# Optimization experiments

Hardware: AMD Instinct MI355X
Metric: run time of the kernel (lower is better)

The kernel has to match this reference:

```python
import jax, jax.numpy as jnp
import numpy as np

N = 100000          # nodes
E = 3200000         # edges
C_IN = 64
HIDDEN = 64
NUM_CLASSES = 10
NUM_GRAPHS = 256
EPS = 1e-5


def _graph_conv(x, src, dst, w_rel, w_root, b):
    # PyG GraphConv(aggr='mean'): out_i = W_rel * mean_{j->i} x_j + W_root * x_i + b
    msg_sum = jax.ops.segment_sum(x[src], dst, num_segments=N)            # [N, C]
    cnt = jax.ops.segment_sum(jnp.ones((src.shape[0], 1), x.dtype), dst,
                              num_segments=N)                             # [N, 1]
    agg = msg_sum / jnp.maximum(cnt, 1.0)
    return agg @ w_rel + x @ w_root + b


def _batch_norm(x, gamma, beta):
    # PyG BatchNorm in training mode: batch stats over the node dimension
    mean = jnp.mean(x, axis=0)
    var = jnp.var(x, axis=0)
    return (x - mean) * jax.lax.rsqrt(var + EPS) * gamma + beta


def setup_inputs() -> dict:
    key = jax.random.key(0)
    ks = jax.random.split(key, 20)
    x = jax.random.normal(ks[0], (N, C_IN), dtype=jnp.float32)
    edge_index = jax.random.randint(ks[1], (2, E), 0, N, dtype=jnp.int32)
    batch = jnp.sort(jax.random.randint(ks[2], (N,), 0, NUM_GRAPHS, dtype=jnp.int32))

    def lin(k, fan_in, fan_out):
        s = 1.0 / np.sqrt(fan_in)
        return jax.random.uniform(k, (fan_in, fan_out), jnp.float32, -s, s)

    dims = [(C_IN, 16), (16, 32), (32, 32), (32, HIDDEN)]
    params = {}
    ki = 3
    for i, (ci, co) in enumerate(dims, start=1):
        params[f"w_rel{i}"] = lin(ks[ki], ci, co); ki += 1
        params[f"w_root{i}"] = lin(ks[ki], ci, co); ki += 1
        params[f"b{i}"] = jnp.zeros((co,), jnp.float32)
        params[f"g{i}"] = jnp.ones((co,), jnp.float32)
        params[f"be{i}"] = jnp.zeros((co,), jnp.float32)
    params["w_lin1"] = lin(ks[ki], HIDDEN, HIDDEN); ki += 1
    params["b_lin1"] = jnp.zeros((HIDDEN,), jnp.float32)
    params["w_lin2"] = lin(ks[ki], HIDDEN, NUM_CLASSES); ki += 1
    params["b_lin2"] = jnp.zeros((NUM_CLASSES,), jnp.float32)

    return {"x": x, "edge_index": edge_index, "batch": batch, **params}


def reference(x, edge_index, batch,
              w_rel1, w_root1, b1, g1, be1,
              w_rel2, w_root2, b2, g2, be2,
              w_rel3, w_root3, b3, g3, be3,
              w_rel4, w_root4, b4, g4, be4,
              w_lin1, b_lin1, w_lin2, b_lin2):
    src, dst = edge_index[0], edge_index[1]
    h = jax.nn.elu(_batch_norm(_graph_conv(x, src, dst, w_rel1, w_root1, b1), g1, be1))
    h = jax.nn.elu(_batch_norm(_graph_conv(h, src, dst, w_rel2, w_root2, b2), g2, be2))
    h = jax.nn.elu(_batch_norm(_graph_conv(h, src, dst, w_rel3, w_root3, b3), g3, be3))
    h = jax.nn.elu(_batch_norm(_graph_conv(h, src, dst, w_rel4, w_root4, b4), g4, be4))
    # global mean pool over graphs
    pooled = jax.ops.segment_sum(h, batch, num_segments=NUM_GRAPHS)
    cnt = jax.ops.segment_sum(jnp.ones((N, 1), h.dtype), batch, num_segments=NUM_GRAPHS)
    pooled = pooled / jnp.maximum(cnt, 1.0)
    z = jax.nn.relu(pooled @ w_lin1 + b_lin1)
    # dropout omitted (deterministic / eval mode)
    logits = z @ w_lin2 + b_lin2
    return jax.nn.log_softmax(logits, axis=-1)
```

## Files before the change

### kernel.cpp

```cpp
#include <hip/hip_runtime.h>
#include <hip/hip_bf16.h>
#include <math.h>

#define NGRAPHS 256
#define BSHIFT 8
#define NBUCK 512
#define NSORT 256
#define LSTAT 1024
#define GCHUNK 1024
#define SMASK 0x00FFFFFFu

__device__ __forceinline__ float bf2f(unsigned short u) {
    return __uint_as_float((unsigned)u << 16);
}
__device__ __forceinline__ unsigned short f2bf(float f) {
    unsigned u = __float_as_uint(f);
    unsigned r = (u + 0x7FFFu + ((u >> 16) & 1u)) >> 16;
    return (unsigned short)r;
}

__global__ __launch_bounds__(256) void k_bhist(const int* __restrict__ dst, int* __restrict__ hmat, int E,
                                               const float* __restrict__ x, const float* __restrict__ w_rel1,
                                               unsigned short* __restrict__ y1b,
                                               int* __restrict__ colpos, int N) {
    int bid = blockIdx.x, tid = threadIdx.x;
    if (bid < NSORT) {
        __shared__ int hist[NBUCK];
        for (int i = tid; i < NBUCK; i += 256) hist[i] = 0;
        __syncthreads();
        int chunk = (E + NSORT - 1) / NSORT;
        int lo = bid * chunk;
        int hi = lo + chunk; if (hi > E) hi = E;
        for (int i = lo + tid; i < hi; i += 256)
            atomicAdd(&hist[__builtin_nontemporal_load(dst + i) >> BSHIFT], 1);
        __syncthreads();
        for (int i = tid; i < NBUCK; i += 256) {
            int h = hist[i];
            int base = atomicAdd(&colpos[i], h);
            hmat[(size_t)bid * NBUCK + i] = base;
        }
    } else {
        __shared__ float s_rel[64 * 16];
        for (int i = tid; i < 64 * 16; i += 256) s_rel[i] = w_rel1[i];
        __syncthreads();
        int total = N * 4;
        int nb = gridDim.x - NSORT;
        for (int i = (bid - NSORT) * 256 + tid; i < total; i += nb * 256) {
            int n = i >> 2, c0 = (i & 3) << 2;
            const float4* mp = (const float4*)(x + (size_t)n * 64);
            float4 acc; acc.x = 0.f; acc.y = 0.f; acc.z = 0.f; acc.w = 0.f;
#pragma unroll
            for (int k2 = 0; k2 < 16; k2++) {
                float4 v = mp[k2];
                const float* wr = &s_rel[(k2 * 4) * 16 + c0];
                float4 w0 = *(const float4*)(wr);
                float4 w1 = *(const float4*)(wr + 16);
                float4 w2 = *(const float4*)(wr + 32);
                float4 w3 = *(const float4*)(wr + 48);
                acc.x += v.x * w0.x + v.y * w1.x + v.z * w2.x + v.w * w3.x;
                acc.y += v.x * w0.y + v.y * w1.y + v.z * w2.y + v.w * w3.y;
                acc.z += v.x * w0.z + v.y * w1.z + v.z * w2.z + v.w * w3.z;
                acc.w += v.x * w0.w + v.y * w1.w + v.z * w2.w + v.w * w3.w;
            }
            ushort4 o; o.x = f2bf(acc.x); o.y = f2bf(acc.y); o.z = f2bf(acc.z); o.w = f2bf(acc.w);
            *(ushort4*)(y1b + (size_t)n * 16 + c0) = o;
        }
    }
}

__global__ __launch_bounds__(512) void k_bscatter(const int* __restrict__ src, const int* __restrict__ dst,
                                                  const int* __restrict__ hmat, const int* __restrict__ colpos,
                                                  int* __restrict__ bstart_g,
                                                  unsigned* __restrict__ ebuf, int E) {
    __shared__ int s[NBUCK];
    __shared__ int cur[NBUCK];
    int tid = threadIdx.x;
    int b = blockIdx.x;
    int v = colpos[tid];
    s[tid] = v;
    __syncthreads();
    for (int off = 1; off < NBUCK; off <<= 1) {
        int t = (tid >= off) ? s[tid - off] : 0;
        __syncthreads();
        s[tid] += t;
        __syncthreads();
    }
    int excl = s[tid] - v;
    if (b == 0) {
        bstart_g[tid] = excl;
        if (tid == NBUCK - 1) bstart_g[NBUCK] = s[NBUCK - 1];
    }
    cur[tid] = excl + hmat[(size_t)b * NBUCK + tid];
    __syncthreads();
    int chunk = (E + NSORT - 1) / NSORT;
    int lo = b * chunk;
    int hi = lo + chunk; if (hi > E) hi = E;
    for (int i = lo + tid; i < hi; i += 512) {
        int d = __builtin_nontemporal_load(dst + i);
        int sv = __builtin_nontemporal_load(src + i);
        int p = atomicAdd(&cur[d >> BSHIFT], 1);
        ebuf[p] = (unsigned)sv | ((unsigned)(d & 255) << 24);
    }
}

__global__ __launch_bounds__(256) void k_sort2(const unsigned* __restrict__ ebuf, const int* __restrict__ bstart,
                                               int* __restrict__ csr, int* __restrict__ row_start, int N) {
    __shared__ int hist[256];
    __shared__ int sc[256];
    __shared__ int scur[256];
    int b = blockIdx.x;
    int e0 = bstart[b], e1 = bstart[b + 1];
    hist[threadIdx.x] = 0;
    __syncthreads();
    for (int i = e0 + threadIdx.x; i < e1; i += 256)
        atomicAdd(&hist[__builtin_nontemporal_load(ebuf + i) >> 24], 1);
    __syncthreads();
    sc[threadIdx.x] = hist[threadIdx.x];
    __syncthreads();
    for (int off = 1; off < 256; off <<= 1) {
        int t = (threadIdx.x >= off) ? sc[threadIdx.x - off] : 0;
        __syncthreads();
        sc[threadIdx.x] += t;
        __syncthreads();
    }
    {
        int inc = sc[threadIdx.x];
        int ex = inc - hist[threadIdx.x];
        scur[threadIdx.x] = e0 + ex;
        int node = (b << BSHIFT) + threadIdx.x;
        if (node < N) row_start[node] = e0 + ex;
        if (node == N - 1) row_start[N] = e0 + inc;
    }
    __syncthreads();
    for (int i = e0 + threadIdx.x; i < e1; i += 256) {
        unsigned w = __builtin_nontemporal_load(ebuf + i);
        int p = atomicAdd(&scur[w >> 24], 1);
        csr[p] = (int)(w & SMASK);
    }
}

template <int C>
__global__ __launch_bounds__(256) void k_gather(const unsigned short* __restrict__ h,
                                                const int* __restrict__ row_start,
                                                const int* __restrict__ csr, float* __restrict__ agg, int N) {
    constexpr int LPR = C / 4;
    constexpr int EPP = 64 / LPR;
    constexpr int BATCH = 4 * EPP;
    __shared__ int sbuf[GCHUNK];
    int lane = threadIdx.x & 63;
    int w = threadIdx.x >> 6;
    int nb = blockIdx.x * 4;
    int wid = nb + w;
    bool act = wid < N;
    int nb_end = nb + 4; if (nb_end > N) nb_end = N;
    int eb0 = row_start[nb];
    int eb1 = row_start[nb_end];
    int r0 = act ? row_start[wid] : 0;
    int r1 = act ? row_start[wid + 1] : 0;
    int es = lane / LPR;
    int cq = (lane % LPR) * 4;

    float a0 = 0.f, a1 = 0.f, a2 = 0.f, a3 = 0.f;
    for (int base = eb0; base < eb1; base += GCHUNK) {
        int len = eb1 - base; if (len > GCHUNK) len = GCHUNK;
        __syncthreads();
        for (int i = threadIdx.x; i < len; i += 256)
            sbuf[i] = __builtin_nontemporal_load(csr + base + i);
        __syncthreads();
        if (act) {
            int lo = (r0 > base ? r0 : base) - base;
            int hiv = r1 < base + len ? r1 : base + len;
            int hi = hiv - base;
            for (int j0 = lo; j0 < hi; j0 += BATCH) {
                int s[4]; bool p[4];
#pragma unroll
                for (int u = 0; u < 4; u++) {
                    int j = j0 + u * EPP + es;
                    p[u] = j < hi;
                    s[u] = sbuf[p[u] ? j : j0];
                }
                ushort4 v[4];
#pragma unroll
                for (int u = 0; u < 4; u++)
                    v[u] = *(const ushort4*)(h + (size_t)s[u] * C + cq);
#pragma unroll
                for (int u = 0; u < 4; u++) {
                    if (p[u]) {
                        a0 += bf2f(v[u].x); a1 += bf2f(v[u].y);
                        a2 += bf2f(v[u].z); a3 += bf2f(v[u].w);
                    }
                }
            }
        }
    }
#pragma unroll
    for (int off = LPR; off < 64; off <<= 1) {
        a0 += __shfl_xor(a0, off, 64);
        a1 += __shfl_xor(a1, off, 64);
        a2 += __shfl_xor(a2, off, 64);
        a3 += __shfl_xor(a3, off, 64);
    }
    if (act && lane < LPR) {
        int deg = r1 - r0;
        float rec = 1.0f / (float)(deg > 0 ? deg : 1);
        float4 o; o.x = a0 * rec; o.y = a1 * rec; o.z = a2 * rec; o.w = a3 * rec;
        *(float4*)(agg + (size_t)wid * C + cq) = o;
    }
}

template <int CI, int CO, bool HAS_REL, bool ADD_AGG, bool IN_BF16>
__global__ __launch_bounds__(256) void k_lin_stats(const void* __restrict__ hroot_v, const float* __restrict__ hrel,
                                                   const float* __restrict__ w_rel, const float* __restrict__ w_root,
                                                   const float* __restrict__ bias,
                                                   float* __restrict__ out, float* __restrict__ gsl, int N) {
    constexpr int QPR = CO / 4;
    __shared__ float s_rel[HAS_REL ? CI * CO : 1];
    __shared__ float s_root[CI * CO];
    __shared__ float s_b[CO];
    __shared__ float part[4][2 * CO];
    int tid = threadIdx.x;
    if (HAS_REL)
        for (int i = tid; i < CI * CO; i += 256) s_rel[i] = w_rel[i];
    for (int i = tid; i < CI * CO; i += 256) s_root[i] = w_root[i];
    if (tid < CO) s_b[tid] = bias[tid];
    __syncthreads();

    int total = N * QPR;
    int stride = gridDim.x * 256;
    float s0 = 0, s1 = 0, s2 = 0, s3 = 0, q0 = 0, q1 = 0, q2 = 0, q3 = 0;
    for (int i = blockIdx.x * 256 + tid; i < total; i += stride) {
        int n = i / QPR, c0 = (i % QPR) * 4;
        float4 acc = *(const float4*)&s_b[c0];
        if (ADD_AGG) {
            float4 v = ((const float4*)hrel)[i];
            acc.x += v.x; acc.y += v.y; acc.z += v.z; acc.w += v.w;
        }
#pragma unroll
        for (int cb = 0; cb < CI / 4; cb++) {
            float f0, f1, f2, f3;
            if (IN_BF16) {
                ushort4 v = *(const ushort4*)((const unsigned short*)hroot_v + (size_t)n * CI + cb * 4);
                f0 = bf2f(v.x); f1 = bf2f(v.y); f2 = bf2f(v.z); f3 = bf2f(v.w);
            } else {
                float4 v = *(const float4*)((const float*)hroot_v + (size_t)n * CI + cb * 4);
                f0 = v.x; f1 = v.y; f2 = v.z; f3 = v.w;
            }
            const float* wr = &s_root[(cb * 4) * CO + c0];
            float4 w0 = *(const float4*)(wr);
            float4 w1 = *(const float4*)(wr + CO);
            float4 w2 = *(const float4*)(wr + 2 * CO);
            float4 w3 = *(const float4*)(wr + 3 * CO);
            acc.x += f0 * w0.x + f1 * w1.x + f2 * w2.x + f3 * w3.x;
            acc.y += f0 * w0.y + f1 * w1.y + f2 * w2.y + f3 * w3.y;
            acc.z += f0 * w0.z + f1 * w1.z + f2 * w2.z + f3 * w3.z;
            acc.w += f0 * w0.w + f1 * w1.w + f2 * w2.w + f3 * w3.w;
            if (HAS_REL) {
                float4 a = *(const float4*)(hrel + (size_t)n * CI + cb * 4);
                const float* we = &s_rel[(cb * 4) * CO + c0];
                float4 e0 = *(const float4*)(we);
                float4 e1 = *(const float4*)(we + CO);
                float4 e2 = *(const float4*)(we + 2 * CO);
                float4 e3 = *(const float4*)(we + 3 * CO);
                acc.x += a.x * e0.x + a.y * e1.x + a.z * e2.x + a.w * e3.x;
                acc.y += a.x * e0.y + a.y * e1.y + a.z * e2.y + a.w * e3.y;
                acc.z += a.x * e0.z + a.y * e1.z + a.z * e2.z + a.w * e3.z;
                acc.w += a.x * e0.w + a.y * e1.w + a.z * e2.w + a.w * e3.w;
            }
        }
        ((float4*)out)[i] = acc;
        s0 += acc.x; q0 += acc.x * acc.x;
        s1 += acc.y; q1 += acc.y * acc.y;
        s2 += acc.z; q2 += acc.z * acc.z;
        s3 += acc.w; q3 += acc.w * acc.w;
    }
#pragma unroll
    for (int off = QPR; off < 64; off <<= 1) {
        s0 += __shfl_xor(s0, off, 64); q0 += __shfl_xor(q0, off, 64);
        s1 += __shfl_xor(s1, off, 64); q1 += __shfl_xor(q1, off, 64);
        s2 += __shfl_xor(s2, off, 64); q2 += __shfl_xor(q2, off, 64);
        s3 += __shfl_xor(s3, off, 64); q3 += __shfl_xor(q3, off, 64);
    }
    int lane = tid & 63;
    int w = tid >> 6;
    if (lane < QPR) {
        int cq = lane * 4;
        part[w][cq + 0] = s0; part[w][CO + cq + 0] = q0;
        part[w][cq + 1] = s1; part[w][CO + cq + 1] = q1;
        part[w][cq + 2] = s2; part[w][CO + cq + 2] = q2;
        part[w][cq + 3] = s3; part[w][CO + cq + 3] = q3;
    }
    __syncthreads();
    if (tid < 2 * CO) {
        float v = part[0][tid] + part[1][tid] + part[2][tid] + part[3][tid];
        atomicAdd(&gsl[tid], v);
    }
}

template <int CO>
__global__ __launch_bounds__(256) void k_bn_elu(const float* __restrict__ h, const float* __restrict__ gsl,
                                                const float* __restrict__ g, const float* __restrict__ be,
                                                unsigned short* __restrict__ hb, float invN, int N) {
    __shared__ float sc[CO], sh[CO];
    if (threadIdx.x < CO) {
        int c = threadIdx.x;
        float mean = gsl[c] * invN;
        float var = gsl[CO + c] * invN - mean * mean;
        float s = g[c] * rsqrtf(var + 1e-5f);
        sc[c] = s;
        sh[c] = be[c] - mean * s;
    }
    __syncthreads();
    int total = N * (CO / 4);
    int i = blockIdx.x * 256 + threadIdx.x;
    if (i >= total) return;
    float4 v = ((const float4*)h)[i];
    int cq = (i % (CO / 4)) * 4;
    v.x = v.x * sc[cq + 0] + sh[cq + 0];
    v.y = v.y * sc[cq + 1] + sh[cq + 1];
    v.z = v.z * sc[cq + 2] + sh[cq + 2];
    v.w = v.w * sc[cq + 3] + sh[cq + 3];
    v.x = v.x > 0.f ? v.x : expm1f(v.x);
    v.y = v.y > 0.f ? v.y : expm1f(v.y);
    v.z = v.z > 0.f ? v.z : expm1f(v.z);
    v.w = v.w > 0.f ? v.w : expm1f(v.w);
    ushort4 o;
    o.x = f2bf(v.x); o.y = f2bf(v.y); o.z = f2bf(v.z); o.w = f2bf(v.w);
    ((ushort4*)hb)[i] = o;
}

__global__ __launch_bounds__(256) void k_bn_elu_pool(const float* __restrict__ h, const float* __restrict__ gsl,
                                                     const float* __restrict__ g, const float* __restrict__ be,
                                                     const int* __restrict__ batch,
                                                     float* __restrict__ pooled, float* __restrict__ cntg,
                                                     float invN, int N) {
    __shared__ float sc[64], sh[64];
    if (threadIdx.x < 64) {
        int c = threadIdx.x;
        float mean = gsl[c] * invN;
        float var = gsl[64 + c] * invN - mean * mean;
        float s = g[c] * rsqrtf(var + 1e-5f);
        sc[c] = s;
        sh[c] = be[c] - mean * s;
    }
    __syncthreads();
    int lane = threadIdx.x & 63;
    int wid = blockIdx.x * 4 + (threadIdx.x >> 6);
    int n0 = wid * 16;
    if (n0 >= N) return;
    float scl = sc[lane];
    float shl = sh[lane];
    int nmax = N - n0; if (nmax > 16) nmax = 16;
    int cur = batch[n0];
    float acc = 0.f;
    float run = 0.f;
    for (int k = 0; k < nmax; k++) {
        int gg = batch[n0 + k];
        if (gg != cur) {
            atomicAdd(&pooled[(size_t)cur * 64 + lane], acc);
            if (lane == 0) atomicAdd(&cntg[cur], run);
            cur = gg; acc = 0.f; run = 0.f;
        }
        float v = h[(size_t)(n0 + k) * 64 + lane] * scl + shl;
        v = v > 0.f ? v : expm1f(v);
        acc += v;
        run += 1.f;
    }
    atomicAdd(&pooled[(size_t)cur * 64 + lane], acc);
    if (lane == 0) atomicAdd(&cntg[cur], run);
}

__global__ __launch_bounds__(256) void k_head(const float* __restrict__ pooled, const float* __restrict__ cntg,
                                              const float* __restrict__ w1, const float* __restrict__ b1,
                                              const float* __restrict__ w2, const float* __restrict__ b2,
                                              float* __restrict__ out) {
    int g = threadIdx.x;
    float rec = 1.0f / fmaxf(cntg[g], 1.0f);
    float p[64];
    {
        const float4* pp = (const float4*)(pooled + (size_t)g * 64);
#pragma unroll
        for (int i = 0; i < 16; i++) {
            float4 v = pp[i];
            p[4 * i + 0] = v.x * rec; p[4 * i + 1] = v.y * rec;
            p[4 * i + 2] = v.z * rec; p[4 * i + 3] = v.w * rec;
        }
    }
    float lg[10];
#pragma unroll
    for (int t = 0; t < 10; t++) lg[t] = b2[t];
#pragma unroll 1
    for (int j = 0; j < 64; j++) {
        float a = b1[j];
#pragma unroll
        for (int k = 0; k < 64; k++) a += p[k] * w1[k * 64 + j];
        a = fmaxf(a, 0.f);
#pragma unroll
        for (int t = 0; t < 10; t++) lg[t] += a * w2[j * 10 + t];
    }
    float m = -1e30f;
#pragma unroll
    for (int t = 0; t < 10; t++) m = fmaxf(m, lg[t]);
    float s = 0.f;
#pragma unroll
    for (int t = 0; t < 10; t++) s += expf(lg[t] - m);
    float lse = m + logf(s);
#pragma unroll
    for (int t = 0; t < 10; t++) out[(size_t)g * 10 + t] = lg[t] - lse;
}

extern "C" void kernel_launch(void* const* d_in, const int* in_sizes, int n_in,
                              void* d_out, int out_size, void* d_ws, size_t ws_size,
                              hipStream_t stream) {
    const float* x = (const float*)d_in[0];
    const int* ei = (const int*)d_in[1];
    const int* batch = (const int*)d_in[2];
    const int N = in_sizes[0] / 64;
    const int E = in_sizes[1] / 2;
    const int* src = ei;
    const int* dst = ei + E;

    const float* w_rel1 = (const float*)d_in[3];
    const float* w_root1 = (const float*)d_in[4];
    const float* b1 = (const float*)d_in[5];
    const float* g1 = (const float*)d_in[6];
    const float* be1 = (const float*)d_in[7];
    const float* w_rel2 = (const float*)d_in[8];
    const float* w_root2 = (const float*)d_in[9];
    const float* b2 = (const float*)d_in[10];
    const float* g2 = (const float*)d_in[11];
    const float* be2 = (const float*)d_in[12];
    const float* w_rel3 = (const float*)d_in[13];
    const float* w_root3 = (const float*)d_in[14];
    const float* b3 = (const float*)d_in[15];
    const float* g3 = (const float*)d_in[16];
    const float* be3 = (const float*)d_in[17];
    const float* w_rel4 = (const float*)d_in[18];
    const float* w_root4 = (const float*)d_in[19];
    const float* b4 = (const float*)d_in[20];
    const float* g4 = (const float*)d_in[21];
    const float* be4 = (const float*)d_in[22];
    const float* w_lin1 = (const float*)d_in[23];
    const float* b_lin1 = (const float*)d_in[24];
    const float* w_lin2 = (const float*)d_in[25];
    const float* b_lin2 = (const float*)d_in[26];

    char* ws = (char*)d_ws;
    size_t off = 0;
    auto alloc = [&](size_t bytes) { size_t o = off; off += (bytes + 255) & ~(size_t)255; return o; };
    int* hmat = (int*)(ws + alloc((size_t)NSORT * NBUCK * 4));
    int* bstart = (int*)(ws + alloc((size_t)(NBUCK + 1) * 4));
    unsigned* ebuf = (unsigned*)(ws + alloc((size_t)E * 4));
    int* csr = (int*)(ws + alloc((size_t)E * 4));
    int* row_start = (int*)(ws + alloc((size_t)(N + 1) * 4));
    float* agg = (float*)(ws + alloc((size_t)N * 32 * 4));
    unsigned short* y1b = (unsigned short*)(ws + alloc((size_t)N * 16 * 2));
    unsigned short* hb = (unsigned short*)(ws + alloc((size_t)N * 64 * 2));
    float* bufA = (float*)(ws + alloc((size_t)N * 64 * 4));
    const int zwords = NBUCK + 512 + NGRAPHS * 64 + NGRAPHS;
    int* colpos = (int*)(ws + alloc((size_t)zwords * 4));
    float* gs = (float*)(colpos + NBUCK);
    float* pooled = gs + 512;
    float* cntg = pooled + NGRAPHS * 64;

    hipMemsetAsync(colpos, 0, (size_t)zwords * 4, stream);

    const float invN = 1.0f / (float)N;
    const int gbl = (N + 3) / 4;

    k_bhist<<<1024, 256, 0, stream>>>(dst, hmat, E, x, w_rel1, y1b, colpos, N);
    k_bscatter<<<NSORT, 512, 0, stream>>>(src, dst, hmat, colpos, bstart, ebuf, E);
    k_sort2<<<NBUCK, 256, 0, stream>>>(ebuf, bstart, csr, row_start, N);

    k_gather<16><<<gbl, 256, 0, stream>>>(y1b, row_start, csr, agg, N);
    k_lin_stats<64, 16, false, true, false><<<LSTAT, 256, 0, stream>>>(
        x, agg, nullptr, w_root1, b1, bufA, gs + 0, N);
    k_bn_elu<16><<<(N * 4 + 255) / 256, 256, 0, stream>>>(bufA, gs + 0, g1, be1, hb, invN, N);

    k_gather<16><<<gbl, 256, 0, stream>>>(hb, row_start, csr, agg, N);
    k_lin_stats<16, 32, true, false, true><<<LSTAT, 256, 0, stream>>>(
        hb, agg, w_rel2, w_root2, b2, bufA, gs + 128, N);
    k_bn_elu<32><<<(N * 8 + 255) / 256, 256, 0, stream>>>(bufA, gs + 128, g2, be2, hb, invN, N);

    k_gather<32><<<gbl, 256, 0, stream>>>(hb, row_start, csr, agg, N);
    k_lin_stats<32, 32, true, false, true><<<LSTAT, 256, 0, stream>>>(
        hb, agg, w_rel3, w_root3, b3, bufA, gs + 256, N);
    k_bn_elu<32><<<(N * 8 + 255) / 256, 256, 0, stream>>>(bufA, gs + 256, g3, be3, hb, invN, N);

    k_gather<32><<<gbl, 256, 0, stream>>>(hb, row_start, csr, agg, N);
    k_lin_stats<32, 64, true, false, true><<<LSTAT, 256, 0, stream>>>(
        hb, agg, w_rel4, w_root4, b4, bufA, gs + 384, N);
    int waves16 = (N + 15) / 16;
    k_bn_elu_pool<<<(waves16 + 3) / 4, 256, 0, stream>>>(
        bufA, gs + 384, g4, be4, batch, pooled, cntg, invN, N);

    k_head<<<1, 256, 0, stream>>>(pooled, cntg, w_lin1, b_lin1, w_lin2, b_lin2, (float*)d_out);
}
```

Before: 589.5 us.

## Overlap root linear transform with neighbor gather in a combined launch

The root-term matmul (x @ W_root + b) moves out of the post-gather linear kernel into extra blocks appended to the gather launch, so it runs concurrently with the memory-bound neighbor aggregation. The follow-up kernel now only adds the rel-term (or the aggregate) to the precomputed output and accumulates batch-norm statistics. The aim is to hide the root compute and its input reads behind the gather. In exchange, bufA is written and then read back and rewritten, adding traffic, and the root blocks compete with gather blocks for CUs.

```diff
diff --git a/kernel.cpp b/kernel.cpp
--- a/kernel.cpp
+++ b/kernel.cpp
@@ -6,6 +6,7 @@
 #define BSHIFT 8
 #define NBUCK 512
 #define NSORT 256
+#define RB 512
 #define LSTAT 1024
 #define GCHUNK 1024
 #define SMASK 0x00FFFFFFu
@@ -139,123 +140,140 @@
     }
 }
 
-template <int C>
-__global__ __launch_bounds__(256) void k_gather(const unsigned short* __restrict__ h,
-                                                const int* __restrict__ row_start,
-                                                const int* __restrict__ csr, float* __restrict__ agg, int N) {
-    constexpr int LPR = C / 4;
+template <int CI, int CIR, int CO, bool ROOT_F32>
+__global__ __launch_bounds__(256) void k_gather_root(const unsigned short* __restrict__ hsrc,
+                                                     const void* __restrict__ hroot_v,
+                                                     const int* __restrict__ row_start, const int* __restrict__ csr,
+                                                     float* __restrict__ agg,
+                                                     const float* __restrict__ w_root, const float* __restrict__ bias,
+                                                     float* __restrict__ out, int N, int gbl) {
+    constexpr int LPR = CI / 4;
     constexpr int EPP = 64 / LPR;
     constexpr int BATCH = 4 * EPP;
+    constexpr int QPR = CO / 4;
     __shared__ int sbuf[GCHUNK];
-    int lane = threadIdx.x & 63;
-    int w = threadIdx.x >> 6;
-    int nb = blockIdx.x * 4;
-    int wid = nb + w;
-    bool act = wid < N;
-    int nb_end = nb + 4; if (nb_end > N) nb_end = N;
-    int eb0 = row_start[nb];
-    int eb1 = row_start[nb_end];
-    int r0 = act ? row_start[wid] : 0;
-    int r1 = act ? row_start[wid + 1] : 0;
-    int es = lane / LPR;
-    int cq = (lane % LPR) * 4;
-
-    float a0 = 0.f, a1 = 0.f, a2 = 0.f, a3 = 0.f;
-    for (int base = eb0; base < eb1; base += GCHUNK) {
-        int len = eb1 - base; if (len > GCHUNK) len = GCHUNK;
-        __syncthreads();
-        for (int i = threadIdx.x; i < len; i += 256)
-            sbuf[i] = __builtin_nontemporal_load(csr + base + i);
-        __syncthreads();
-        if (act) {
-            int lo = (r0 > base ? r0 : base) - base;
-            int hiv = r1 < base + len ? r1 : base + len;
-            int hi = hiv - base;
-            for (int j0 = lo; j0 < hi; j0 += BATCH) {
-                int s[4]; bool p[4];
-#pragma unroll
-                for (int u = 0; u < 4; u++) {
-                    int j = j0 + u * EPP + es;
-                    p[u] = j < hi;
-                    s[u] = sbuf[p[u] ? j : j0];
-                }
-                ushort4 v[4];
-#pragma unroll
-                for (int u = 0; u < 4; u++)
-                    v[u] = *(const ushort4*)(h + (size_t)s[u] * C + cq);
-#pragma unroll
-                for (int u = 0; u < 4; u++) {
-                    if (p[u]) {
-                        a0 += bf2f(v[u].x); a1 += bf2f(v[u].y);
-                        a2 += bf2f(v[u].z); a3 += bf2f(v[u].w);
+    __shared__ float s_root[CIR * CO];
+    __shared__ float s_b[CO];
+    int tid = threadIdx.x;
+
+    if ((int)blockIdx.x < gbl) {
+        int lane = tid & 63;
+        int w = tid >> 6;
+        int nb = blockIdx.x * 4;
+        int wid = nb + w;
+        bool act = wid < N;
+        int nb_end = nb + 4; if (nb_end > N) nb_end = N;
+        int eb0 = row_start[nb];
+        int eb1 = row_start[nb_end];
+        int r0 = act ? row_start[wid] : 0;
+        int r1 = act ? row_start[wid + 1] : 0;
+        int es = lane / LPR;
+        int cq = (lane % LPR) * 4;
+
+        float a0 = 0.f, a1 = 0.f, a2 = 0.f, a3 = 0.f;
+        for (int base = eb0; base < eb1; base += GCHUNK) {
+            int len = eb1 - base; if (len > GCHUNK) len = GCHUNK;
+            __syncthreads();
+            for (int i = tid; i < len; i += 256)
+                sbuf[i] = __builtin_nontemporal_load(csr + base + i);
+            __syncthreads();
+            if (act) {
+                int lo = (r0 > base ? r0 : base) - base;
+                int hiv = r1 < base + len ? r1 : base + len;
+                int hi = hiv - base;
+                for (int j0 = lo; j0 < hi; j0 += BATCH) {
+                    int s[4]; bool p[4];
+#pragma unroll
+                    for (int u = 0; u < 4; u++) {
+                        int j = j0 + u * EPP + es;
+                        p[u] = j < hi;
+                        s[u] = sbuf[p[u] ? j : j0];
+                    }
+                    ushort4 v[4];
+#pragma unroll
+                    for (int u = 0; u < 4; u++)
+                        v[u] = *(const ushort4*)(hsrc + (size_t)s[u] * CI + cq);
+#pragma unroll
+                    for (int u = 0; u < 4; u++) {
+                        if (p[u]) {
+                            a0 += bf2f(v[u].x); a1 += bf2f(v[u].y);
+                            a2 += bf2f(v[u].z); a3 += bf2f(v[u].w);
+                        }
                     }
                 }
             }
         }
-    }
-#pragma unroll
-    for (int off = LPR; off < 64; off <<= 1) {
-        a0 += __shfl_xor(a0, off, 64);
-        a1 += __shfl_xor(a1, off, 64);
-        a2 += __shfl_xor(a2, off, 64);
-        a3 += __shfl_xor(a3, off, 64);
-    }
-    if (act && lane < LPR) {
-        int deg = r1 - r0;
-        float rec = 1.0f / (float)(deg > 0 ? deg : 1);
-        float4 o; o.x = a0 * rec; o.y = a1 * rec; o.z = a2 * rec; o.w = a3 * rec;
-        *(float4*)(agg + (size_t)wid * C + cq) = o;
-    }
-}
-
-template <int CI, int CO, bool HAS_REL, bool ADD_AGG, bool IN_BF16>
-__global__ __launch_bounds__(256) void k_lin_stats(const void* __restrict__ hroot_v, const float* __restrict__ hrel,
-                                                   const float* __restrict__ w_rel, const float* __restrict__ w_root,
-                                                   const float* __restrict__ bias,
-                                                   float* __restrict__ out, float* __restrict__ gsl, int N) {
+#pragma unroll
+        for (int off = LPR; off < 64; off <<= 1) {
+            a0 += __shfl_xor(a0, off, 64);
+            a1 += __shfl_xor(a1, off, 64);
+            a2 += __shfl_xor(a2, off, 64);
+            a3 += __shfl_xor(a3, off, 64);
+        }
+        if (act && lane < LPR) {
+            int deg = r1 - r0;
+            float rec = 1.0f / (float)(deg > 0 ? deg : 1);
+            float4 o; o.x = a0 * rec; o.y = a1 * rec; o.z = a2 * rec; o.w = a3 * rec;
+            *(float4*)(agg + (size_t)wid * CI + cq) = o;
+        }
+    } else {
+        int rb = blockIdx.x - gbl;
+        for (int i = tid; i < CIR * CO; i += 256) s_root[i] = w_root[i];
+        if (tid < CO) s_b[tid] = bias[tid];
+        __syncthreads();
+        int total = N * QPR;
+        for (int i = rb * 256 + tid; i < total; i += RB * 256) {
+            int n = i / QPR, c0 = (i % QPR) * 4;
+            float4 acc = *(const float4*)&s_b[c0];
+#pragma unroll
+            for (int cb = 0; cb < CIR / 4; cb++) {
+                float f0, f1, f2, f3;
+                if (ROOT_F32) {
+                    float4 v = *(const float4*)((const float*)hroot_v + (size_t)n * CIR + cb * 4);
+                    f0 = v.x; f1 = v.y; f2 = v.z; f3 = v.w;
+                } else {
+                    ushort4 v = *(const ushort4*)((const unsigned short*)hroot_v + (size_t)n * CIR + cb * 4);
+                    f0 = bf2f(v.x); f1 = bf2f(v.y); f2 = bf2f(v.z); f3 = bf2f(v.w);
+                }
+                const float* wr = &s_root[(cb * 4) * CO + c0];
+                float4 w0 = *(const float4*)(wr);
+                float4 w1 = *(const float4*)(wr + CO);
+                float4 w2 = *(const float4*)(wr + 2 * CO);
+                float4 w3 = *(const float4*)(wr + 3 * CO);
+                acc.x += f0 * w0.x + f1 * w1.x + f2 * w2.x + f3 * w3.x;
+                acc.y += f0 * w0.y + f1 * w1.y + f2 * w2.y + f3 * w3.y;
+                acc.z += f0 * w0.z + f1 * w1.z + f2 * w2.z + f3 * w3.z;
+                acc.w += f0 * w0.w + f1 * w1.w + f2 * w2.w + f3 * w3.w;
+            }
+            ((float4*)out)[i] = acc;
+        }
+    }
+}
+
+template <int CI, int CO, bool HAS_REL>
+__global__ __launch_bounds__(256) void k_aggstats(const float* __restrict__ agg, const float* __restrict__ w_rel,
+                                                  float* __restrict__ inout, float* __restrict__ gsl, int N) {
     constexpr int QPR = CO / 4;
     __shared__ float s_rel[HAS_REL ? CI * CO : 1];
-    __shared__ float s_root[CI * CO];
-    __shared__ float s_b[CO];
     __shared__ float part[4][2 * CO];
     int tid = threadIdx.x;
     if (HAS_REL)
         for (int i = tid; i < CI * CO; i += 256) s_rel[i] = w_rel[i];
-    for (int i = tid; i < CI * CO; i += 256) s_root[i] = w_root[i];
-    if (tid < CO) s_b[tid] = bias[tid];
     __syncthreads();
 
     int total = N * QPR;
     int stride = gridDim.x * 256;
     float s0 = 0, s1 = 0, s2 = 0, s3 = 0, q0 = 0, q1 = 0, q2 = 0, q3 = 0;
     for (int i = blockIdx.x * 256 + tid; i < total; i += stride) {
-        int n = i / QPR, c0 = (i % QPR) * 4;
-        float4 acc = *(const float4*)&s_b[c0];
-        if (ADD_AGG) {
-            float4 v = ((const float4*)hrel)[i];
+        float4 acc = ((const float4*)inout)[i];
+        if (!HAS_REL) {
+            float4 v = ((const float4*)agg)[i];
             acc.x += v.x; acc.y += v.y; acc.z += v.z; acc.w += v.w;
-        }
-#pragma unroll
-        for (int cb = 0; cb < CI / 4; cb++) {
-            float f0, f1, f2, f3;
-            if (IN_BF16) {
-                ushort4 v = *(const ushort4*)((const unsigned short*)hroot_v + (size_t)n * CI + cb * 4);
-                f0 = bf2f(v.x); f1 = bf2f(v.y); f2 = bf2f(v.z); f3 = bf2f(v.w);
-            } else {
-                float4 v = *(const float4*)((const float*)hroot_v + (size_t)n * CI + cb * 4);
-                f0 = v.x; f1 = v.y; f2 = v.z; f3 = v.w;
-            }
-            const float* wr = &s_root[(cb * 4) * CO + c0];
-            float4 w0 = *(const float4*)(wr);
-            float4 w1 = *(const float4*)(wr + CO);
-            float4 w2 = *(const float4*)(wr + 2 * CO);
-            float4 w3 = *(const float4*)(wr + 3 * CO);
-            acc.x += f0 * w0.x + f1 * w1.x + f2 * w2.x + f3 * w3.x;
-            acc.y += f0 * w0.y + f1 * w1.y + f2 * w2.y + f3 * w3.y;
-            acc.z += f0 * w0.z + f1 * w1.z + f2 * w2.z + f3 * w3.z;
-            acc.w += f0 * w0.w + f1 * w1.w + f2 * w2.w + f3 * w3.w;
-            if (HAS_REL) {
-                float4 a = *(const float4*)(hrel + (size_t)n * CI + cb * 4);
+        } else {
+            int n = i / QPR, c0 = (i % QPR) * 4;
+#pragma unroll
+            for (int cb = 0; cb < CI / 4; cb++) {
+                float4 a = *(const float4*)(agg + (size_t)n * CI + cb * 4);
                 const float* we = &s_rel[(cb * 4) * CO + c0];
                 float4 e0 = *(const float4*)(we);
                 float4 e1 = *(const float4*)(we + CO);
@@ -267,7 +285,7 @@
                 acc.w += a.x * e0.w + a.y * e1.w + a.z * e2.w + a.w * e3.w;
             }
         }
-        ((float4*)out)[i] = acc;
+        ((float4*)inout)[i] = acc;
         s0 += acc.x; q0 += acc.x * acc.x;
         s1 += acc.y; q1 += acc.y * acc.y;
         s2 += acc.z; q2 += acc.z * acc.z;
@@ -471,24 +489,24 @@
     k_bscatter<<<NSORT, 512, 0, stream>>>(src, dst, hmat, colpos, bstart, ebuf, E);
     k_sort2<<<NBUCK, 256, 0, stream>>>(ebuf, bstart, csr, row_start, N);
 
-    k_gather<16><<<gbl, 256, 0, stream>>>(y1b, row_start, csr, agg, N);
-    k_lin_stats<64, 16, false, true, false><<<LSTAT, 256, 0, stream>>>(
-        x, agg, nullptr, w_root1, b1, bufA, gs + 0, N);
+    k_gather_root<16, 64, 16, true><<<gbl + RB, 256, 0, stream>>>(
+        y1b, x, row_start, csr, agg, w_root1, b1, bufA, N, gbl);
+    k_aggstats<16, 16, false><<<LSTAT, 256, 0, stream>>>(agg, nullptr, bufA, gs + 0, N);
     k_bn_elu<16><<<(N * 4 + 255) / 256, 256, 0, stream>>>(bufA, gs + 0, g1, be1, hb, invN, N);
 
-    k_gather<16><<<gbl, 256, 0, stream>>>(hb, row_start, csr, agg, N);
-    k_lin_stats<16, 32, true, false, true><<<LSTAT, 256, 0, stream>>>(
-        hb, agg, w_rel2, w_root2, b2, bufA, gs + 128, N);
+    k_gather_root<16, 16, 32, false><<<gbl + RB, 256, 0, stream>>>(
+        hb, hb, row_start, csr, agg, w_root2, b2, bufA, N, gbl);
+    k_aggstats<16, 32, true><<<LSTAT, 256, 0, stream>>>(agg, w_rel2, bufA, gs + 128, N);
     k_bn_elu<32><<<(N * 8 + 255) / 256, 256, 0, stream>>>(bufA, gs + 128, g2, be2, hb, invN, N);
 
-    k_gather<32><<<gbl, 256, 0, stream>>>(hb, row_start, csr, agg, N);
-    k_lin_stats<32, 32, true, false, true><<<LSTAT, 256, 0, stream>>>(
-        hb, agg, w_rel3, w_root3, b3, bufA, gs + 256, N);
+    k_gather_root<32, 32, 32, false><<<gbl + RB, 256, 0, stream>>>(
+        hb, hb, row_start, csr, agg, w_root3, b3, bufA, N, gbl);
+    k_aggstats<32, 32, true><<<LSTAT, 256, 0, stream>>>(agg, w_rel3, bufA, gs + 256, N);
     k_bn_elu<32><<<(N * 8 + 255) / 256, 256, 0, stream>>>(bufA, gs + 256, g3, be3, hb, invN, N);
 
-    k_gather<32><<<gbl, 256, 0, stream>>>(hb, row_start, csr, agg, N);
-    k_lin_stats<32, 64, true, false, true><<<LSTAT, 256, 0, stream>>>(
-        hb, agg, w_rel4, w_root4, b4, bufA, gs + 384, N);
+    k_gather_root<32, 32, 64, false><<<gbl + RB, 256, 0, stream>>>(
+        hb, hb, row_start, csr, agg, w_root4, b4, bufA, N, gbl);
+    k_aggstats<32, 64, true><<<LSTAT, 256, 0, stream>>>(agg, w_rel4, bufA, gs + 384, N);
     int waves16 = (N + 15) / 16;
     k_bn_elu_pool<<<(waves16 + 3) / 4, 256, 0, stream>>>(
         bufA, gs + 384, g4, be4, batch, pooled, cntg, invN, N);
```

After: 652.0 us. 1.11x slower.
